# Optimization experiments

Measured on AMD Instinct MI355X. Metric: run time of the kernel, lower is better.

## Reference

```python
import jax, jax.numpy as jnp
import numpy as np

B, N, C, F, E, K = 2, 2048, 1024, 4096, 8, 2

def setup_inputs() -> dict:
    key = jax.random.key(0)
    k = jax.random.split(key, 6)
    xavier1 = float(np.sqrt(6.0 / (C + F)))
    xavier2 = float(np.sqrt(6.0 / (F + C)))
    return {
        "x": jax.random.normal(k[0], (B, N, C), dtype=jnp.float32),
        "router_w": jax.random.normal(k[1], (E, C), dtype=jnp.float32) * 0.01,
        "w1": jax.random.uniform(k[2], (E, F, C), dtype=jnp.float32, minval=-xavier1, maxval=xavier1),
        "b1": jnp.zeros((E, F), dtype=jnp.float32),
        "w2": jax.random.uniform(k[3], (E, C, F), dtype=jnp.float32, minval=-xavier2, maxval=xavier2),
        "b2": jnp.zeros((E, C), dtype=jnp.float32),
    }

def reference(x, router_w, w1, b1, w2, b2):
    Bb, Nn, Cc = x.shape
    x_flat = x.reshape(-1, Cc)                                   # [T, C]
    # Router (eval mode: no noise)
    logits = jnp.einsum('tc,ec->te', x_flat, router_w)           # [T, E]
    probs = jax.nn.softmax(logits, axis=-1)
    top_w, top_idx = jax.lax.top_k(probs, K)                     # [T, K]
    top_w = top_w / (jnp.sum(top_w, axis=-1, keepdims=True) + 1e-9)
    # Dense all-expert MLP (same math as the per-expert gather/scatter loop)
    h = jnp.einsum('tc,efc->tef', x_flat, w1) + b1[None]          # [T, E, F]
    h = jax.nn.relu(h)
    y = jnp.einsum('tef,ecf->tec', h, w2) + b2[None]              # [T, E, C]
    # Gather the K selected experts per token and combine
    sel = jnp.take_along_axis(y, top_idx[:, :, None], axis=1)    # [T, K, C]
    out = jnp.einsum('tkc,tk->tc', sel, top_w)                   # [T, C]
    return out.reshape(Bb, Nn, Cc)
```

## Files before the change

### kernel.cpp

```cpp
#include <hip/hip_runtime.h>
#include <hip/hip_fp16.h>


#define T_TOK 4096
#define C_DIM 1024
#define F_DIM 4096
#define E_NUM 8
#define MAXT 80
#define NP   (MAXT * 128)
#define TILE_H 8192

typedef float f32x4 __attribute__((ext_vector_type(4)));
typedef _Float16 half8 __attribute__((ext_vector_type(8)));
typedef _Float16 half4 __attribute__((ext_vector_type(4)));

#define AS1 __attribute__((address_space(1)))
#define AS3 __attribute__((address_space(3)))

__device__ __forceinline__ int swz(int r, int ec) { return ec ^ ((r & 7) << 3); }

__device__ __forceinline__ half8 cvt8(float4 f0, float4 f1) {
  half8 hv;
  hv[0] = (_Float16)f0.x; hv[1] = (_Float16)f0.y; hv[2] = (_Float16)f0.z; hv[3] = (_Float16)f0.w;
  hv[4] = (_Float16)f1.x; hv[5] = (_Float16)f1.y; hv[6] = (_Float16)f1.z; hv[7] = (_Float16)f1.w;
  return hv;
}

__device__ __forceinline__ int xcd_swz(int bid, int nwg) {
  int xcd = bid & 7, rest = bid >> 3;
  int q = nwg >> 3, r = nwg & 7;
  return (xcd < r ? xcd * (q + 1) : r * (q + 1) + (xcd - r) * q) + rest;
}

__global__ __launch_bounds__(256) void router_kernel(
    const float* __restrict__ x, const float* __restrict__ rw,
    int* __restrict__ top_idx, float* __restrict__ top_w)
{
  int t = blockIdx.x * 4 + (threadIdx.x >> 6);
  int lane = threadIdx.x & 63;
  const float* xr = x + (size_t)t * C_DIM;
  float acc[E_NUM];
#pragma unroll
  for (int e = 0; e < E_NUM; ++e) acc[e] = 0.f;
  for (int j = 0; j < C_DIM / 64; ++j) {
    int c = j * 64 + lane;
    float xv = xr[c];
#pragma unroll
    for (int e = 0; e < E_NUM; ++e) acc[e] += xv * rw[e * C_DIM + c];
  }
#pragma unroll
  for (int e = 0; e < E_NUM; ++e) {
    float v = acc[e];
#pragma unroll
    for (int off = 32; off > 0; off >>= 1) v += __shfl_xor(v, off);
    acc[e] = v;
  }
  if (lane == 0) {
    float mx = acc[0];
    for (int e = 1; e < E_NUM; ++e) mx = fmaxf(mx, acc[e]);
    float p[E_NUM]; float Z = 0.f;
    for (int e = 0; e < E_NUM; ++e) { p[e] = expf(acc[e] - mx); Z += p[e]; }
    int b0 = 0;
    for (int e = 1; e < E_NUM; ++e) if (p[e] > p[b0]) b0 = e;
    int b1i = -1; float pb = -1.f;
    for (int e = 0; e < E_NUM; ++e) if (e != b0 && p[e] > pb) { pb = p[e]; b1i = e; }
    float p0 = p[b0] / Z, p1 = pb / Z;
    float s = p0 + p1 + 1e-9f;
    top_idx[t * 2 + 0] = b0;
    top_idx[t * 2 + 1] = b1i;
    top_w[t * 2 + 0] = p0 / s;
    top_w[t * 2 + 1] = p1 / s;
  }
}

__global__ void build_lists(const int* __restrict__ top_idx,
                            int* __restrict__ rows_g, int* __restrict__ counts,
                            int* __restrict__ tile_off, int* __restrict__ inv)
{
  int e = threadIdx.x >> 6;
  int lane = threadIdx.x & 63;
  int cnt = 0;
  for (int t0 = 0; t0 < T_TOK; t0 += 64) {
    int t = t0 + lane;
    bool sel = (top_idx[t * 2] == e) || (top_idx[t * 2 + 1] == e);
    cnt += __popcll(__ballot(sel));
  }
  if (lane == 0) counts[e] = cnt;
  __syncthreads();
  if (threadIdx.x == 0) {
    int o = 0;
    for (int i = 0; i < E_NUM; ++i) { tile_off[i] = o; o += 2 * ((counts[i] + 255) >> 8); }
    tile_off[E_NUM] = o;
  }
  __syncthreads();
  int base = tile_off[e] * 128;
  int pos = 0;
  for (int t0 = 0; t0 < T_TOK; t0 += 64) {
    int t = t0 + lane;
    int i0 = top_idx[t * 2], i1 = top_idx[t * 2 + 1];
    bool sel = (i0 == e) || (i1 == e);
    unsigned long long mask = __ballot(sel);
    if (sel) {
      int p = pos + __popcll(mask & ((1ull << lane) - 1ull));
      int slot = t * 2 + ((i0 == e) ? 0 : 1);
      rows_g[base + p] = slot;
      inv[slot] = (e << 16) | (base + p);
    }
    pos += __popcll(mask);
  }
}

__global__ __launch_bounds__(256) void gather_x(
    const float* __restrict__ x, const int* __restrict__ rows_g,
    const int* __restrict__ counts, const int* __restrict__ tile_off,
    _Float16* __restrict__ xg)
{
  unsigned g = blockIdx.x * 256 + threadIdx.x;
  unsigned p = g >> 7, ccr = g & 127;
  int gt = p >> 7, r = p & 127;
  int kc = ccr >> 3, c8 = ccr & 7;
  int e = -1;
#pragma unroll
  for (int i = 0; i < E_NUM; ++i)
    if (gt >= tile_off[i] && gt < tile_off[i + 1]) e = i;
  half8 hv = {};
  if (e >= 0) {
    int nrem = counts[e] - (gt - tile_off[e]) * 128;
    if (r < nrem) {
      int t = rows_g[p] >> 1;
      const float4* s = reinterpret_cast<const float4*>(x + (size_t)t * C_DIM + kc * 64 + c8 * 8);
      hv = cvt8(s[0], s[1]);
    }
  }
  *reinterpret_cast<half8*>(xg + ((size_t)gt * 16 + kc) * TILE_H + r * 64 + ((c8 ^ (r & 7)) << 3)) = hv;
}

__global__ __launch_bounds__(256) void cvt_w(
    const float* __restrict__ w1, const float* __restrict__ w2,
    _Float16* __restrict__ w1t, _Float16* __restrict__ w2t,
    int ch, int Fc, int lgnftl, int lgnkc, unsigned halfChunks)
{
  unsigned g = blockIdx.x * 256 + threadIdx.x;
  if (g < halfChunks) {
    unsigned tile = g >> 10;
    unsigned kc = tile & 15;
    unsigned et = tile >> 4;
    unsigned ftl = et & ((1u << lgnftl) - 1);
    unsigned e = et >> lgnftl;
    unsigned r = (g >> 3) & 127;
    unsigned sc = g & 7;
    unsigned c8 = sc ^ (r & 7);
    unsigned frow = ftl * 128 + r;
    const float4* s = reinterpret_cast<const float4*>(
        w1 + ((size_t)e * F_DIM + ch * Fc + frow) * C_DIM + kc * 64 + c8 * 8);
    *reinterpret_cast<half8*>(w1t + (size_t)g * 8) = cvt8(s[0], s[1]);
  } else {
    unsigned g2 = g - halfChunks;
    unsigned tile = g2 >> 10;
    unsigned kc = tile & ((1u << lgnkc) - 1);
    unsigned et = tile >> lgnkc;
    unsigned ct = et & 7;
    unsigned e = et >> 3;
    unsigned r = (g2 >> 3) & 127;
    unsigned sc = g2 & 7;
    unsigned c8 = sc ^ (r & 7);
    unsigned c = ct * 128 + r;
    const float4* s = reinterpret_cast<const float4*>(
        w2 + ((size_t)e * C_DIM + c) * F_DIM + ch * Fc + kc * 64 + c8 * 8);
    *reinterpret_cast<half8*>(w2t + (size_t)g2 * 8) = cvt8(s[0], s[1]);
  }
}

#define LDS_T(buf_, ix_) (lds + ((size_t)((buf_) * 4 + (ix_))) * TILE_H)

#define STAGE4(buf_, a0_, a1_, b0_, b1_)                                          \
  {                                                                               \
    _Pragma("unroll")                                                             \
    for (int i_ = 0; i_ < 2; ++i_) {                                              \
      int o_ = tid * 8 + i_ * 4096;                                               \
      __builtin_amdgcn_global_load_lds((const AS1 void*)((a0_) + o_),             \
          (AS3 void*)(LDS_T(buf_, 0) + o_), 16, 0, 0);                            \
      __builtin_amdgcn_global_load_lds((const AS1 void*)((a1_) + o_),             \
          (AS3 void*)(LDS_T(buf_, 1) + o_), 16, 0, 0);                            \
      __builtin_amdgcn_global_load_lds((const AS1 void*)((b0_) + o_),             \
          (AS3 void*)(LDS_T(buf_, 2) + o_), 16, 0, 0);                            \
      __builtin_amdgcn_global_load_lds((const AS1 void*)((b1_) + o_),             \
          (AS3 void*)(LDS_T(buf_, 3) + o_), 16, 0, 0);                            \
    }                                                                             \
  }

#define COMPUTE256(buf_)                                                          \
  _Pragma("unroll")                                                               \
  for (int kk = 0; kk < 64; kk += 32) {                                           \
    const int klo = kk + (lane >> 4) * 8;                                         \
    half8 aF[8], bF[4];                                                           \
    const _Float16* aT_ = LDS_T(buf_, wr);                                        \
    const _Float16* bT_ = LDS_T(buf_, 2 + (wc >> 1));                             \
    _Pragma("unroll")                                                             \
    for (int m = 0; m < 8; ++m) {                                                 \
      int r = m * 16 + (lane & 15);                                               \
      aF[m] = *reinterpret_cast<const half8*>(&aT_[r * 64 + swz(r, klo)]);        \
    }                                                                             \
    _Pragma("unroll")                                                             \
    for (int n = 0; n < 4; ++n) {                                                 \
      int rb = (wc & 1) * 64 + n * 16 + (lane & 15);                              \
      bF[n] = *reinterpret_cast<const half8*>(&bT_[rb * 64 + swz(rb, klo)]);      \
    }                                                                             \
    _Pragma("unroll")                                                             \
    for (int m = 0; m < 8; ++m)                                                   \
      _Pragma("unroll")                                                           \
      for (int n = 0; n < 4; ++n)                                                 \
        acc[m][n] = __builtin_amdgcn_mfma_f32_16x16x32_f16(bF[n], aF[m], acc[m][n], 0, 0, 0); \
  }

__global__ __launch_bounds__(512, 2) void gemm1_kernel(
    const _Float16* __restrict__ xg, const _Float16* __restrict__ w1t,
    const float* __restrict__ b1, const int* __restrict__ tile_off,
    _Float16* __restrict__ ht, int ch, int Fc)
{
  extern __shared__ _Float16 lds[];
  const int NFT = Fc >> 8;
  const int GBf = (NFT < 4) ? NFT : 4;
  const int perg = 8 * GBf;
  const int ngrpF = NFT / GBf;
  const int wgid = xcd_swz(blockIdx.x, gridDim.x);
  const int grp = wgid / perg;
  const int inner = wgid - grp * perg;
  const int ftq = inner % GBf;
  const int gp = inner / GBf;
  const int gtg = grp / ngrpF;
  const int ftg = grp - gtg * ngrpF;
  const int ft = ftg * GBf + ftq;
  const int gt = (gtg * 8 + gp) * 2;
  if (gt >= tile_off[E_NUM]) return;
  int e = 0;
  while (gt >= tile_off[e + 1]) ++e;
  const int nftl = Fc >> 7;
  const _Float16* At0 = xg + (size_t)gt * 16 * TILE_H;
  const _Float16* At1 = xg + (size_t)(gt + 1) * 16 * TILE_H;
  const _Float16* Bt0 = w1t + (size_t)(e * nftl + 2 * ft) * 16 * TILE_H;
  const _Float16* Bt1 = w1t + (size_t)(e * nftl + 2 * ft + 1) * 16 * TILE_H;

  const int tid = threadIdx.x;
  const int lane = tid & 63;
  const int wave = tid >> 6;
  const int wr = wave >> 2, wc = wave & 3;

  f32x4 acc[8][4];
#pragma unroll
  for (int m = 0; m < 8; ++m)
#pragma unroll
    for (int n = 0; n < 4; ++n) acc[m][n] = (f32x4){0.f, 0.f, 0.f, 0.f};

  STAGE4(0, At0, At1, Bt0, Bt1);
  __syncthreads();
  for (int kc = 0; kc < 16; ++kc) {
    const int cur = kc & 1;
    if (kc + 1 < 16) {
      size_t ko = (size_t)(kc + 1) * TILE_H;
      STAGE4(cur ^ 1, At0 + ko, At1 + ko, Bt0 + ko, Bt1 + ko);
    }
    COMPUTE256(cur);
    __syncthreads();
  }

  const int nkcF = Fc >> 6;
  const int gtw = gt + wr;
  const float* b1e = b1 + e * F_DIM + ch * Fc;
#pragma unroll
  for (int m = 0; m < 8; ++m) {
    int tok = m * 16 + (lane & 15);
#pragma unroll
    for (int n = 0; n < 4; ++n) {
      int flb = ft * 256 + wc * 64 + n * 16 + ((lane >> 4) << 2);
      float4 bv = *reinterpret_cast<const float4*>(b1e + flb);
      half4 hv;
      hv[0] = (_Float16)fmaxf(acc[m][n][0] + bv.x, 0.f);
      hv[1] = (_Float16)fmaxf(acc[m][n][1] + bv.y, 0.f);
      hv[2] = (_Float16)fmaxf(acc[m][n][2] + bv.z, 0.f);
      hv[3] = (_Float16)fmaxf(acc[m][n][3] + bv.w, 0.f);
      *reinterpret_cast<half4*>(
          ht + ((size_t)gtw * nkcF + (flb >> 6)) * TILE_H + tok * 64 +
          ((((flb >> 3) & 7) ^ (tok & 7)) << 3) + (flb & 7)) = hv;
    }
  }
}

__global__ __launch_bounds__(512, 2) void gemm2_kernel(
    const _Float16* __restrict__ ht, const _Float16* __restrict__ w2t,
    const int* __restrict__ tile_off, _Float16* __restrict__ y,
    int Fc, int kspl, int accum)
{
  extern __shared__ _Float16 lds[];
  const int NGT2 = MAXT / 2;
  const int wgid = xcd_swz(blockIdx.x, gridDim.x);
  const int ks = wgid / (NGT2 * 4);
  const int r0 = wgid - ks * NGT2 * 4;
  const int grp8 = r0 >> 5;
  const int inner = r0 & 31;
  const int ct2 = inner & 3;
  const int gp = inner >> 2;
  const int gt = (grp8 * 8 + gp) * 2;
  if (gt >= tile_off[E_NUM]) return;
  int e = 0;
  while (gt >= tile_off[e + 1]) ++e;
  const int nkc = Fc >> 6;
  const int klen = nkc / kspl;
  const _Float16* At0 = ht + ((size_t)gt * nkc + ks * klen) * TILE_H;
  const _Float16* At1 = ht + ((size_t)(gt + 1) * nkc + ks * klen) * TILE_H;
  const _Float16* Bt0 = w2t + ((size_t)(e * 8 + 2 * ct2) * nkc + ks * klen) * TILE_H;
  const _Float16* Bt1 = w2t + ((size_t)(e * 8 + 2 * ct2 + 1) * nkc + ks * klen) * TILE_H;

  const int tid = threadIdx.x;
  const int lane = tid & 63;
  const int wave = tid >> 6;
  const int wr = wave >> 2, wc = wave & 3;

  f32x4 acc[8][4];
#pragma unroll
  for (int m = 0; m < 8; ++m)
#pragma unroll
    for (int n = 0; n < 4; ++n) acc[m][n] = (f32x4){0.f, 0.f, 0.f, 0.f};

  STAGE4(0, At0, At1, Bt0, Bt1);
  __syncthreads();
  for (int kc = 0; kc < klen; ++kc) {
    const int cur = kc & 1;
    if (kc + 1 < klen) {
      size_t ko = (size_t)(kc + 1) * TILE_H;
      STAGE4(cur ^ 1, At0 + ko, At1 + ko, Bt0 + ko, Bt1 + ko);
    }
    COMPUTE256(cur);
    __syncthreads();
  }

  _Float16* yk = y + ((size_t)(ks * MAXT + gt + wr) * 128) * C_DIM;
#pragma unroll
  for (int m = 0; m < 8; ++m) {
    int tok = m * 16 + (lane & 15);
#pragma unroll
    for (int n = 0; n < 4; ++n) {
      int cb = ct2 * 256 + wc * 64 + n * 16 + ((lane >> 4) << 2);
      half4* p = reinterpret_cast<half4*>(yk + (size_t)tok * C_DIM + cb);
      half4 hv;
      if (accum) {
        half4 old = *p;
        hv[0] = (_Float16)(acc[m][n][0] + (float)old[0]);
        hv[1] = (_Float16)(acc[m][n][1] + (float)old[1]);
        hv[2] = (_Float16)(acc[m][n][2] + (float)old[2]);
        hv[3] = (_Float16)(acc[m][n][3] + (float)old[3]);
      } else {
        hv[0] = (_Float16)acc[m][n][0];
        hv[1] = (_Float16)acc[m][n][1];
        hv[2] = (_Float16)acc[m][n][2];
        hv[3] = (_Float16)acc[m][n][3];
      }
      *p = hv;
    }
  }
}

__global__ __launch_bounds__(256) void combine_kernel(
    const _Float16* __restrict__ y, const int* __restrict__ inv,
    const float* __restrict__ top_w, const float* __restrict__ b2,
    float* __restrict__ out, int kspl)
{
  int g = blockIdx.x * 256 + threadIdx.x;
  int t = g >> 7, c8 = (g & 127) << 3;
  float o[8];
#pragma unroll
  for (int i = 0; i < 8; ++i) o[i] = 0.f;
#pragma unroll
  for (int k = 0; k < 2; ++k) {
    int iv = inv[t * 2 + k];
    int e = iv >> 16, pos = iv & 0xffff;
    float w = top_w[t * 2 + k];
    const float4* bb = reinterpret_cast<const float4*>(b2 + e * C_DIM + c8);
    float4 bv0 = bb[0], bv1 = bb[1];
    float s[8] = {bv0.x, bv0.y, bv0.z, bv0.w, bv1.x, bv1.y, bv1.z, bv1.w};
    for (int ks = 0; ks < kspl; ++ks) {
      half8 hv = *reinterpret_cast<const half8*>(
          y + ((size_t)(ks * MAXT * 128 + pos)) * C_DIM + c8);
#pragma unroll
      for (int i = 0; i < 8; ++i) s[i] += (float)hv[i];
    }
#pragma unroll
    for (int i = 0; i < 8; ++i) o[i] += w * s[i];
  }
  float4* op = reinterpret_cast<float4*>(out + (size_t)t * C_DIM + c8);
  op[0] = (float4){o[0], o[1], o[2], o[3]};
  op[1] = (float4){o[4], o[5], o[6], o[7]};
}

extern "C" void kernel_launch(void* const* d_in, const int* in_sizes, int n_in,
                              void* d_out, int out_size, void* d_ws, size_t ws_size,
                              hipStream_t stream)
{
  const float* x  = (const float*)d_in[0];
  const float* rw = (const float*)d_in[1];
  const float* w1 = (const float*)d_in[2];
  const float* b1 = (const float*)d_in[3];
  const float* w2 = (const float*)d_in[4];
  const float* b2 = (const float*)d_in[5];
  float* out = (float*)d_out;

  char* ws = (char*)d_ws;
  size_t off = 0;
  auto carve = [&](size_t bytes) -> void* {
    void* p = ws + off;
    off += (bytes + 255) & ~(size_t)255;
    return p;
  };
  int*   top_idx  = (int*)carve((size_t)T_TOK * 2 * sizeof(int));
  float* top_w    = (float*)carve((size_t)T_TOK * 2 * sizeof(float));
  int*   counts   = (int*)carve(E_NUM * sizeof(int));
  int*   tile_off = (int*)carve((E_NUM + 1) * sizeof(int));
  int*   rows_g   = (int*)carve((size_t)NP * sizeof(int));
  int*   inv      = (int*)carve((size_t)T_TOK * 2 * sizeof(int));
  _Float16* xg    = (_Float16*)carve((size_t)MAXT * 16 * TILE_H * sizeof(_Float16));
  _Float16* y     = (_Float16*)carve((size_t)4 * NP * C_DIM * sizeof(_Float16));
  size_t fixed = off;

  int nchunk = 8;
  const int cands[4] = {1, 2, 4, 8};
  for (int ci = 0; ci < 4; ++ci) {
    int n = cands[ci];
    size_t fc = (size_t)(F_DIM / n);
    size_t w1b = ((size_t)E_NUM * fc * C_DIM * 2 + 255) & ~(size_t)255;
    size_t w2b = ((size_t)E_NUM * C_DIM * fc * 2 + 255) & ~(size_t)255;
    size_t htb = ((size_t)MAXT * (fc >> 6) * TILE_H * 2 + 255) & ~(size_t)255;
    if (fixed + w1b + w2b + htb <= ws_size) { nchunk = n; break; }
  }
  const int Fc = F_DIM / nchunk;
  int lgFc = 0; while ((1 << lgFc) < Fc) ++lgFc;
  _Float16* w1t = (_Float16*)carve((size_t)E_NUM * Fc * C_DIM * sizeof(_Float16));
  _Float16* w2t = (_Float16*)carve((size_t)E_NUM * C_DIM * Fc * sizeof(_Float16));
  _Float16* ht  = (_Float16*)carve((size_t)MAXT * (Fc >> 6) * TILE_H * sizeof(_Float16));

  const int kspl = (Fc >= 2048) ? 4 : 2;
  const size_t dynLds = (size_t)8 * TILE_H * sizeof(_Float16);

  router_kernel<<<T_TOK / 4, 256, 0, stream>>>(x, rw, top_idx, top_w);
  build_lists<<<1, 512, 0, stream>>>(top_idx, rows_g, counts, tile_off, inv);
  gather_x<<<(MAXT * 128 * 128) / 256, 256, 0, stream>>>(x, rows_g, counts, tile_off, xg);

  const unsigned halfChunks = (unsigned)Fc << 10;
  for (int ch = 0; ch < nchunk; ++ch) {
    cvt_w<<<8 * Fc, 256, 0, stream>>>(w1, w2, w1t, w2t, ch, Fc, lgFc - 7, lgFc - 6, halfChunks);
    gemm1_kernel<<<(MAXT / 2) * (Fc / 256), 512, dynLds, stream>>>(
        xg, w1t, b1, tile_off, ht, ch, Fc);
    gemm2_kernel<<<(MAXT / 2) * 4 * kspl, 512, dynLds, stream>>>(
        ht, w2t, tile_off, y, Fc, kspl, ch != 0);
  }
  combine_kernel<<<(T_TOK * 128) / 256, 256, 0, stream>>>(y, inv, top_w, b2, out, kspl);
}
```

Before: 361.8 us.

## Split K tiles to 32 and use 4-slot LDS ring with vmcnt waits

```diff
diff --git a/kernel.cpp b/kernel.cpp
--- a/kernel.cpp
+++ b/kernel.cpp
@@ -8,7 +8,7 @@
 #define E_NUM 8
 #define MAXT 80
 #define NP   (MAXT * 128)
-#define TILE_H 8192
+#define SUB_H 4096
 
 typedef float f32x4 __attribute__((ext_vector_type(4)));
 typedef _Float16 half8 __attribute__((ext_vector_type(8)));
@@ -16,8 +16,6 @@
 
 #define AS1 __attribute__((address_space(1)))
 #define AS3 __attribute__((address_space(3)))
-
-__device__ __forceinline__ int swz(int r, int ec) { return ec ^ ((r & 7) << 3); }
 
 __device__ __forceinline__ half8 cvt8(float4 f0, float4 f1) {
   half8 hv;
@@ -118,7 +116,8 @@
   unsigned g = blockIdx.x * 256 + threadIdx.x;
   unsigned p = g >> 7, ccr = g & 127;
   int gt = p >> 7, r = p & 127;
-  int kc = ccr >> 3, c8 = ccr & 7;
+  int kc32 = ccr >> 2, c4d = ccr & 3;
+  int c4s = c4d ^ (r & 3);
   int e = -1;
 #pragma unroll
   for (int i = 0; i < E_NUM; ++i)
@@ -128,83 +127,78 @@
     int nrem = counts[e] - (gt - tile_off[e]) * 128;
     if (r < nrem) {
       int t = rows_g[p] >> 1;
-      const float4* s = reinterpret_cast<const float4*>(x + (size_t)t * C_DIM + kc * 64 + c8 * 8);
+      const float4* s = reinterpret_cast<const float4*>(
+          x + (size_t)t * C_DIM + kc32 * 32 + c4s * 8);
       hv = cvt8(s[0], s[1]);
     }
   }
-  *reinterpret_cast<half8*>(xg + ((size_t)gt * 16 + kc) * TILE_H + r * 64 + ((c8 ^ (r & 7)) << 3)) = hv;
+  *reinterpret_cast<half8*>(xg + ((size_t)gt * 32 + kc32) * SUB_H + r * 32 + (c4d << 3)) = hv;
 }
 
 __global__ __launch_bounds__(256) void cvt_w(
     const float* __restrict__ w1, const float* __restrict__ w2,
     _Float16* __restrict__ w1t, _Float16* __restrict__ w2t,
-    int ch, int Fc, int lgnftl, int lgnkc, unsigned halfChunks)
+    int ch, int Fc, int lgnftl, int lgnkc32, unsigned halfChunks)
 {
   unsigned g = blockIdx.x * 256 + threadIdx.x;
   if (g < halfChunks) {
-    unsigned tile = g >> 10;
-    unsigned kc = tile & 15;
-    unsigned et = tile >> 4;
+    unsigned tile = g >> 9;
+    unsigned kc32 = tile & 31;
+    unsigned et = tile >> 5;
     unsigned ftl = et & ((1u << lgnftl) - 1);
     unsigned e = et >> lgnftl;
-    unsigned r = (g >> 3) & 127;
-    unsigned sc = g & 7;
-    unsigned c8 = sc ^ (r & 7);
+    unsigned r = (g >> 2) & 127;
+    unsigned sc = g & 3;
+    unsigned c4s = sc ^ (r & 3);
     unsigned frow = ftl * 128 + r;
     const float4* s = reinterpret_cast<const float4*>(
-        w1 + ((size_t)e * F_DIM + ch * Fc + frow) * C_DIM + kc * 64 + c8 * 8);
+        w1 + ((size_t)e * F_DIM + ch * Fc + frow) * C_DIM + kc32 * 32 + c4s * 8);
     *reinterpret_cast<half8*>(w1t + (size_t)g * 8) = cvt8(s[0], s[1]);
   } else {
     unsigned g2 = g - halfChunks;
-    unsigned tile = g2 >> 10;
-    unsigned kc = tile & ((1u << lgnkc) - 1);
-    unsigned et = tile >> lgnkc;
+    unsigned tile = g2 >> 9;
+    unsigned kc32 = tile & ((1u << lgnkc32) - 1);
+    unsigned et = tile >> lgnkc32;
     unsigned ct = et & 7;
     unsigned e = et >> 3;
-    unsigned r = (g2 >> 3) & 127;
-    unsigned sc = g2 & 7;
-    unsigned c8 = sc ^ (r & 7);
+    unsigned r = (g2 >> 2) & 127;
+    unsigned sc = g2 & 3;
+    unsigned c4s = sc ^ (r & 3);
     unsigned c = ct * 128 + r;
     const float4* s = reinterpret_cast<const float4*>(
-        w2 + ((size_t)e * C_DIM + c) * F_DIM + ch * Fc + kc * 64 + c8 * 8);
+        w2 + ((size_t)e * C_DIM + c) * F_DIM + ch * Fc + kc32 * 32 + c4s * 8);
     *reinterpret_cast<half8*>(w2t + (size_t)g2 * 8) = cvt8(s[0], s[1]);
   }
 }
 
-#define LDS_T(buf_, ix_) (lds + ((size_t)((buf_) * 4 + (ix_))) * TILE_H)
-
-#define STAGE4(buf_, a0_, a1_, b0_, b1_)                                          \
+#define STAGE32(slot_, a0_, a1_, b0_, b1_)                                        \
   {                                                                               \
-    _Pragma("unroll")                                                             \
-    for (int i_ = 0; i_ < 2; ++i_) {                                              \
-      int o_ = tid * 8 + i_ * 4096;                                               \
-      __builtin_amdgcn_global_load_lds((const AS1 void*)((a0_) + o_),             \
-          (AS3 void*)(LDS_T(buf_, 0) + o_), 16, 0, 0);                            \
-      __builtin_amdgcn_global_load_lds((const AS1 void*)((a1_) + o_),             \
-          (AS3 void*)(LDS_T(buf_, 1) + o_), 16, 0, 0);                            \
-      __builtin_amdgcn_global_load_lds((const AS1 void*)((b0_) + o_),             \
-          (AS3 void*)(LDS_T(buf_, 2) + o_), 16, 0, 0);                            \
-      __builtin_amdgcn_global_load_lds((const AS1 void*)((b1_) + o_),             \
-          (AS3 void*)(LDS_T(buf_, 3) + o_), 16, 0, 0);                            \
-    }                                                                             \
-  }
-
-#define COMPUTE256(buf_)                                                          \
-  _Pragma("unroll")                                                               \
-  for (int kk = 0; kk < 64; kk += 32) {                                           \
-    const int klo = kk + (lane >> 4) * 8;                                         \
+    int o_ = tid * 8;                                                             \
+    __builtin_amdgcn_global_load_lds((const AS1 void*)((a0_) + o_),               \
+        (AS3 void*)(lds + ((slot_) * 4 + 0) * SUB_H + o_), 16, 0, 0);             \
+    __builtin_amdgcn_global_load_lds((const AS1 void*)((a1_) + o_),               \
+        (AS3 void*)(lds + ((slot_) * 4 + 1) * SUB_H + o_), 16, 0, 0);             \
+    __builtin_amdgcn_global_load_lds((const AS1 void*)((b0_) + o_),               \
+        (AS3 void*)(lds + ((slot_) * 4 + 2) * SUB_H + o_), 16, 0, 0);             \
+    __builtin_amdgcn_global_load_lds((const AS1 void*)((b1_) + o_),               \
+        (AS3 void*)(lds + ((slot_) * 4 + 3) * SUB_H + o_), 16, 0, 0);             \
+  }
+
+#define COMPUTE32(slot_)                                                          \
+  {                                                                               \
+    const _Float16* aT_ = lds + (size_t)((slot_) * 4 + wr) * SUB_H;               \
+    const _Float16* bT_ = lds + (size_t)((slot_) * 4 + 2 + (wc >> 1)) * SUB_H;    \
+    const int c4_ = lane >> 4;                                                    \
     half8 aF[8], bF[4];                                                           \
-    const _Float16* aT_ = LDS_T(buf_, wr);                                        \
-    const _Float16* bT_ = LDS_T(buf_, 2 + (wc >> 1));                             \
     _Pragma("unroll")                                                             \
     for (int m = 0; m < 8; ++m) {                                                 \
       int r = m * 16 + (lane & 15);                                               \
-      aF[m] = *reinterpret_cast<const half8*>(&aT_[r * 64 + swz(r, klo)]);        \
+      aF[m] = *reinterpret_cast<const half8*>(&aT_[r * 32 + ((c4_ ^ (r & 3)) << 3)]); \
     }                                                                             \
     _Pragma("unroll")                                                             \
     for (int n = 0; n < 4; ++n) {                                                 \
       int rb = (wc & 1) * 64 + n * 16 + (lane & 15);                              \
-      bF[n] = *reinterpret_cast<const half8*>(&bT_[rb * 64 + swz(rb, klo)]);      \
+      bF[n] = *reinterpret_cast<const half8*>(&bT_[rb * 32 + ((c4_ ^ (rb & 3)) << 3)]); \
     }                                                                             \
     _Pragma("unroll")                                                             \
     for (int m = 0; m < 8; ++m)                                                   \
@@ -212,6 +206,29 @@
       for (int n = 0; n < 4; ++n)                                                 \
         acc[m][n] = __builtin_amdgcn_mfma_f32_16x16x32_f16(bF[n], aF[m], acc[m][n], 0, 0, 0); \
   }
+
+#define WAIT_BAR(cnt_)                                                            \
+  asm volatile("s_waitcnt vmcnt(" #cnt_ ")" ::: "memory");                        \
+  __builtin_amdgcn_sched_barrier(0);                                              \
+  __builtin_amdgcn_s_barrier();                                                   \
+  __builtin_amdgcn_sched_barrier(0);
+
+#define KLOOP(n_)                                                                 \
+  STAGE32(0, At0, At1, Bt0, Bt1);                                                 \
+  STAGE32(1, At0 + SUB_H, At1 + SUB_H, Bt0 + SUB_H, Bt1 + SUB_H);                 \
+  STAGE32(2, At0 + 2 * SUB_H, At1 + 2 * SUB_H, Bt0 + 2 * SUB_H, Bt1 + 2 * SUB_H); \
+  for (int s = 0; s < (n_) - 2; ++s) {                                            \
+    WAIT_BAR(8);                                                                  \
+    COMPUTE32(s & 3);                                                             \
+    if (s + 3 < (n_)) {                                                           \
+      size_t ko_ = (size_t)(s + 3) * SUB_H;                                       \
+      STAGE32((s + 3) & 3, At0 + ko_, At1 + ko_, Bt0 + ko_, Bt1 + ko_);           \
+    }                                                                             \
+  }                                                                               \
+  WAIT_BAR(4);                                                                    \
+  COMPUTE32(((n_) - 2) & 3);                                                      \
+  WAIT_BAR(0);                                                                    \
+  COMPUTE32(((n_) - 1) & 3);
 
 __global__ __launch_bounds__(512, 2) void gemm1_kernel(
     const _Float16* __restrict__ xg, const _Float16* __restrict__ w1t,
@@ -236,10 +253,10 @@
   int e = 0;
   while (gt >= tile_off[e + 1]) ++e;
   const int nftl = Fc >> 7;
-  const _Float16* At0 = xg + (size_t)gt * 16 * TILE_H;
-  const _Float16* At1 = xg + (size_t)(gt + 1) * 16 * TILE_H;
-  const _Float16* Bt0 = w1t + (size_t)(e * nftl + 2 * ft) * 16 * TILE_H;
-  const _Float16* Bt1 = w1t + (size_t)(e * nftl + 2 * ft + 1) * 16 * TILE_H;
+  const _Float16* At0 = xg + (size_t)gt * 32 * SUB_H;
+  const _Float16* At1 = xg + (size_t)(gt + 1) * 32 * SUB_H;
+  const _Float16* Bt0 = w1t + (size_t)(e * nftl + 2 * ft) * 32 * SUB_H;
+  const _Float16* Bt1 = w1t + (size_t)(e * nftl + 2 * ft + 1) * 32 * SUB_H;
 
   const int tid = threadIdx.x;
   const int lane = tid & 63;
@@ -252,19 +269,9 @@
 #pragma unroll
     for (int n = 0; n < 4; ++n) acc[m][n] = (f32x4){0.f, 0.f, 0.f, 0.f};
 
-  STAGE4(0, At0, At1, Bt0, Bt1);
-  __syncthreads();
-  for (int kc = 0; kc < 16; ++kc) {
-    const int cur = kc & 1;
-    if (kc + 1 < 16) {
-      size_t ko = (size_t)(kc + 1) * TILE_H;
-      STAGE4(cur ^ 1, At0 + ko, At1 + ko, Bt0 + ko, Bt1 + ko);
-    }
-    COMPUTE256(cur);
-    __syncthreads();
-  }
-
-  const int nkcF = Fc >> 6;
+  KLOOP(32);
+
+  const int nkc32F = Fc >> 5;
   const int gtw = gt + wr;
   const float* b1e = b1 + e * F_DIM + ch * Fc;
 #pragma unroll
@@ -280,8 +287,8 @@
       hv[2] = (_Float16)fmaxf(acc[m][n][2] + bv.z, 0.f);
       hv[3] = (_Float16)fmaxf(acc[m][n][3] + bv.w, 0.f);
       *reinterpret_cast<half4*>(
-          ht + ((size_t)gtw * nkcF + (flb >> 6)) * TILE_H + tok * 64 +
-          ((((flb >> 3) & 7) ^ (tok & 7)) << 3) + (flb & 7)) = hv;
+          ht + ((size_t)gtw * nkc32F + (flb >> 5)) * SUB_H + tok * 32 +
+          (((((flb >> 3) & 3) ^ (tok & 3))) << 3) + (flb & 7)) = hv;
     }
   }
 }
@@ -304,12 +311,12 @@
   if (gt >= tile_off[E_NUM]) return;
   int e = 0;
   while (gt >= tile_off[e + 1]) ++e;
-  const int nkc = Fc >> 6;
-  const int klen = nkc / kspl;
-  const _Float16* At0 = ht + ((size_t)gt * nkc + ks * klen) * TILE_H;
-  const _Float16* At1 = ht + ((size_t)(gt + 1) * nkc + ks * klen) * TILE_H;
-  const _Float16* Bt0 = w2t + ((size_t)(e * 8 + 2 * ct2) * nkc + ks * klen) * TILE_H;
-  const _Float16* Bt1 = w2t + ((size_t)(e * 8 + 2 * ct2 + 1) * nkc + ks * klen) * TILE_H;
+  const int nkc32 = Fc >> 5;
+  const int klen = nkc32 / kspl;
+  const _Float16* At0 = ht + ((size_t)gt * nkc32 + ks * klen) * SUB_H;
+  const _Float16* At1 = ht + ((size_t)(gt + 1) * nkc32 + ks * klen) * SUB_H;
+  const _Float16* Bt0 = w2t + ((size_t)(e * 8 + 2 * ct2) * nkc32 + ks * klen) * SUB_H;
+  const _Float16* Bt1 = w2t + ((size_t)(e * 8 + 2 * ct2 + 1) * nkc32 + ks * klen) * SUB_H;
 
   const int tid = threadIdx.x;
   const int lane = tid & 63;
@@ -322,17 +329,7 @@
 #pragma unroll
     for (int n = 0; n < 4; ++n) acc[m][n] = (f32x4){0.f, 0.f, 0.f, 0.f};
 
-  STAGE4(0, At0, At1, Bt0, Bt1);
-  __syncthreads();
-  for (int kc = 0; kc < klen; ++kc) {
-    const int cur = kc & 1;
-    if (kc + 1 < klen) {
-      size_t ko = (size_t)(kc + 1) * TILE_H;
-      STAGE4(cur ^ 1, At0 + ko, At1 + ko, Bt0 + ko, Bt1 + ko);
-    }
-    COMPUTE256(cur);
-    __syncthreads();
-  }
+  KLOOP(klen);
 
   _Float16* yk = y + ((size_t)(ks * MAXT + gt + wr) * 128) * C_DIM;
 #pragma unroll
@@ -417,7 +414,7 @@
   int*   tile_off = (int*)carve((E_NUM + 1) * sizeof(int));
   int*   rows_g   = (int*)carve((size_t)NP * sizeof(int));
   int*   inv      = (int*)carve((size_t)T_TOK * 2 * sizeof(int));
-  _Float16* xg    = (_Float16*)carve((size_t)MAXT * 16 * TILE_H * sizeof(_Float16));
+  _Float16* xg    = (_Float16*)carve((size_t)MAXT * 32 * SUB_H * sizeof(_Float16));
   _Float16* y     = (_Float16*)carve((size_t)4 * NP * C_DIM * sizeof(_Float16));
   size_t fixed = off;
 
@@ -428,17 +425,17 @@
     size_t fc = (size_t)(F_DIM / n);
     size_t w1b = ((size_t)E_NUM * fc * C_DIM * 2 + 255) & ~(size_t)255;
     size_t w2b = ((size_t)E_NUM * C_DIM * fc * 2 + 255) & ~(size_t)255;
-    size_t htb = ((size_t)MAXT * (fc >> 6) * TILE_H * 2 + 255) & ~(size_t)255;
+    size_t htb = ((size_t)MAXT * (fc >> 5) * SUB_H * 2 + 255) & ~(size_t)255;
     if (fixed + w1b + w2b + htb <= ws_size) { nchunk = n; break; }
   }
   const int Fc = F_DIM / nchunk;
   int lgFc = 0; while ((1 << lgFc) < Fc) ++lgFc;
   _Float16* w1t = (_Float16*)carve((size_t)E_NUM * Fc * C_DIM * sizeof(_Float16));
   _Float16* w2t = (_Float16*)carve((size_t)E_NUM * C_DIM * Fc * sizeof(_Float16));
-  _Float16* ht  = (_Float16*)carve((size_t)MAXT * (Fc >> 6) * TILE_H * sizeof(_Float16));
+  _Float16* ht  = (_Float16*)carve((size_t)MAXT * (Fc >> 5) * SUB_H * sizeof(_Float16));
 
   const int kspl = (Fc >= 2048) ? 4 : 2;
-  const size_t dynLds = (size_t)8 * TILE_H * sizeof(_Float16);
+  const size_t dynLds = (size_t)16 * SUB_H * sizeof(_Float16);
 
   router_kernel<<<T_TOK / 4, 256, 0, stream>>>(x, rw, top_idx, top_w);
   build_lists<<<1, 512, 0, stream>>>(top_idx, rows_g, counts, tile_off, inv);
@@ -446,7 +443,7 @@
 
   const unsigned halfChunks = (unsigned)Fc << 10;
   for (int ch = 0; ch < nchunk; ++ch) {
-    cvt_w<<<8 * Fc, 256, 0, stream>>>(w1, w2, w1t, w2t, ch, Fc, lgFc - 7, lgFc - 6, halfChunks);
+    cvt_w<<<8 * Fc, 256, 0, stream>>>(w1, w2, w1t, w2t, ch, Fc, lgFc - 7, lgFc - 5, halfChunks);
     gemm1_kernel<<<(MAXT / 2) * (Fc / 256), 512, dynLds, stream>>>(
         xg, w1t, b1, tile_off, ht, ch, Fc);
     gemm2_kernel<<<(MAXT / 2) * 4 * kspl, 512, dynLds, stream>>>(
```

After: 358.7 us. About the same (-0.9%).

## Split K-step into ping-pong phases with barriers and MFMA priority

Applied to the files above, without the earlier changes.

```diff
diff --git a/kernel.cpp b/kernel.cpp
--- a/kernel.cpp
+++ b/kernel.cpp
@@ -189,29 +189,58 @@
     }                                                                             \
   }
 
-#define COMPUTE256(buf_)                                                          \
-  _Pragma("unroll")                                                               \
-  for (int kk = 0; kk < 64; kk += 32) {                                           \
-    const int klo = kk + (lane >> 4) * 8;                                         \
-    half8 aF[8], bF[4];                                                           \
-    const _Float16* aT_ = LDS_T(buf_, wr);                                        \
-    const _Float16* bT_ = LDS_T(buf_, 2 + (wc >> 1));                             \
+#define KPHASE(buf_, kk_, mh_, readB_)                                            \
+  {                                                                               \
+    const int klo_ = (kk_) * 32 + ((lane >> 4) << 3);                             \
+    half8 aF[4];                                                                  \
     _Pragma("unroll")                                                             \
-    for (int m = 0; m < 8; ++m) {                                                 \
-      int r = m * 16 + (lane & 15);                                               \
-      aF[m] = *reinterpret_cast<const half8*>(&aT_[r * 64 + swz(r, klo)]);        \
+    for (int mm = 0; mm < 4; ++mm) {                                              \
+      int r = ((mh_) * 4 + mm) * 16 + (lane & 15);                                \
+      aF[mm] = *reinterpret_cast<const half8*>(                                   \
+          &LDS_T(buf_, wr)[r * 64 + swz(r, klo_)]);                               \
     }                                                                             \
+    if (readB_) {                                                                 \
+      _Pragma("unroll")                                                           \
+      for (int n = 0; n < 4; ++n) {                                               \
+        int rb = (wc & 1) * 64 + n * 16 + (lane & 15);                            \
+        bF[n] = *reinterpret_cast<const half8*>(                                  \
+            &LDS_T(buf_, 2 + (wc >> 1))[rb * 64 + swz(rb, klo_)]);                \
+      }                                                                           \
+    }                                                                             \
+    __builtin_amdgcn_sched_barrier(0);                                            \
+    __builtin_amdgcn_s_barrier();                                                 \
+    __builtin_amdgcn_s_setprio(1);                                                \
     _Pragma("unroll")                                                             \
-    for (int n = 0; n < 4; ++n) {                                                 \
-      int rb = (wc & 1) * 64 + n * 16 + (lane & 15);                              \
-      bF[n] = *reinterpret_cast<const half8*>(&bT_[rb * 64 + swz(rb, klo)]);      \
-    }                                                                             \
-    _Pragma("unroll")                                                             \
-    for (int m = 0; m < 8; ++m)                                                   \
+    for (int mm = 0; mm < 4; ++mm)                                                \
       _Pragma("unroll")                                                           \
       for (int n = 0; n < 4; ++n)                                                 \
-        acc[m][n] = __builtin_amdgcn_mfma_f32_16x16x32_f16(bF[n], aF[m], acc[m][n], 0, 0, 0); \
-  }
+        acc[(mh_) * 4 + mm][n] = __builtin_amdgcn_mfma_f32_16x16x32_f16(          \
+            bF[n], aF[mm], acc[(mh_) * 4 + mm][n], 0, 0, 0);                      \
+    __builtin_amdgcn_s_setprio(0);                                                \
+    __builtin_amdgcn_sched_barrier(0);                                            \
+    __builtin_amdgcn_s_barrier();                                                 \
+  }
+
+#define KSTEP(s_, n_, At0_, At1_, Bt0_, Bt1_)                                     \
+  {                                                                               \
+    const int cur_ = (s_) & 1;                                                    \
+    asm volatile("s_waitcnt vmcnt(0)" ::: "memory");                              \
+    __builtin_amdgcn_sched_barrier(0);                                            \
+    __builtin_amdgcn_s_barrier();                                                 \
+    half8 bF[4];                                                                  \
+    if ((s_) + 1 < (n_)) {                                                        \
+      size_t ko_ = (size_t)((s_) + 1) * TILE_H;                                   \
+      STAGE4(cur_ ^ 1, (At0_) + ko_, (At1_) + ko_, (Bt0_) + ko_, (Bt1_) + ko_);   \
+    }                                                                             \
+    KPHASE(cur_, 0, 0, 1);                                                        \
+    KPHASE(cur_, 0, 1, 0);                                                        \
+    KPHASE(cur_, 1, 0, 1);                                                        \
+    KPHASE(cur_, 1, 1, 0);                                                        \
+  }
+
+#define KLOOP(n_, At0_, At1_, Bt0_, Bt1_)                                         \
+  STAGE4(0, At0_, At1_, Bt0_, Bt1_);                                              \
+  for (int s = 0; s < (n_); ++s) { KSTEP(s, (n_), At0_, At1_, Bt0_, Bt1_); }
 
 __global__ __launch_bounds__(512, 2) void gemm1_kernel(
     const _Float16* __restrict__ xg, const _Float16* __restrict__ w1t,
@@ -252,17 +281,7 @@
 #pragma unroll
     for (int n = 0; n < 4; ++n) acc[m][n] = (f32x4){0.f, 0.f, 0.f, 0.f};
 
-  STAGE4(0, At0, At1, Bt0, Bt1);
-  __syncthreads();
-  for (int kc = 0; kc < 16; ++kc) {
-    const int cur = kc & 1;
-    if (kc + 1 < 16) {
-      size_t ko = (size_t)(kc + 1) * TILE_H;
-      STAGE4(cur ^ 1, At0 + ko, At1 + ko, Bt0 + ko, Bt1 + ko);
-    }
-    COMPUTE256(cur);
-    __syncthreads();
-  }
+  KLOOP(16, At0, At1, Bt0, Bt1);
 
   const int nkcF = Fc >> 6;
   const int gtw = gt + wr;
@@ -322,17 +341,7 @@
 #pragma unroll
     for (int n = 0; n < 4; ++n) acc[m][n] = (f32x4){0.f, 0.f, 0.f, 0.f};
 
-  STAGE4(0, At0, At1, Bt0, Bt1);
-  __syncthreads();
-  for (int kc = 0; kc < klen; ++kc) {
-    const int cur = kc & 1;
-    if (kc + 1 < klen) {
-      size_t ko = (size_t)(kc + 1) * TILE_H;
-      STAGE4(cur ^ 1, At0 + ko, At1 + ko, Bt0 + ko, Bt1 + ko);
-    }
-    COMPUTE256(cur);
-    __syncthreads();
-  }
+  KLOOP(klen, At0, At1, Bt0, Bt1);
 
   _Float16* yk = y + ((size_t)(ks * MAXT + gt + wr) * 128) * C_DIM;
 #pragma unroll
```

Result: slower. 373.6 us (+3.2%).
